# Kernel tuning notes

Measured on AMD Instinct MI355X. Metric: run time of the kernel, lower is better.

Reference implementation:

```python
import jax, jax.numpy as jnp
import numpy as np

TEMP = 0.5  # matches temperature init kwarg
EPS = 1e-12  # F.normalize eps


def _l2norm(x):
    # F.normalize(x, dim=1): x / max(||x||, eps)
    n = jnp.linalg.norm(x, axis=1, keepdims=True)
    return x / jnp.maximum(n, EPS)


def setup_inputs() -> dict:
    key = jax.random.key(0)
    k1, k2 = jax.random.split(key)
    B, D = 4096, 256
    return {
        "x_i": jax.random.normal(k1, (B, D), dtype=jnp.float32),
        "x_j": jax.random.normal(k2, (B, D), dtype=jnp.float32),
    }


def reference(x_i, x_j):
    B = x_i.shape[0]
    z = jnp.concatenate([_l2norm(x_i), _l2norm(x_j)], axis=0)  # [2B, D]
    # cosine similarity of normalized rows == matmul (avoids NxNxD broadcast)
    sim = (z @ z.T) / TEMP  # [2B, 2B]
    idx = jnp.arange(B)
    # diagonals at offsets +B and -B = positive pairs
    pos = jnp.concatenate([sim[idx, idx + B], sim[idx + B, idx]])  # [2B]
    exp_sim = jnp.exp(sim)
    # neg = all off-diagonal entries per row (neg_mask = ~eye(2B))
    exp_neg = exp_sim.sum(axis=1) - jnp.exp(jnp.diagonal(sim))  # [2B]
    exp_pos = jnp.exp(pos)
    loss = -jnp.log(exp_pos / (exp_pos + exp_neg))
    return loss.mean()
```

## Files before the change

### kernel.cpp

```cpp
#include <hip/hip_runtime.h>
#include <hip/hip_bf16.h>

typedef __attribute__((ext_vector_type(8))) short bf16x8;
typedef __attribute__((ext_vector_type(4))) float f32x4;
typedef __attribute__((ext_vector_type(4))) unsigned short ushort4v;

constexpr int BB = 4096;
constexpr int D  = 256;
constexpr int R2 = 8192;
constexpr int NSPLIT = 16;
constexpr int CT = 64;
constexpr int NT = (R2 / NSPLIT) / CT;
constexpr float SQRT2 = 1.41421356237309515f;
constexpr float E2 = 7.38905609893065f;

__device__ __forceinline__ unsigned short f2bf(float f) {
    __hip_bfloat16 h = __float2bfloat16(f);
    return *reinterpret_cast<unsigned short*>(&h);
}

__device__ __forceinline__ void async16(const unsigned short* g, unsigned short* l) {
    __builtin_amdgcn_global_load_lds(
        (const __attribute__((address_space(1))) void*)g,
        (__attribute__((address_space(3))) void*)l,
        16, 0, 0);
}

__global__ __launch_bounds__(256) void norm_kernel(const float* __restrict__ xi,
                                                   const float* __restrict__ xj,
                                                   unsigned short* __restrict__ z,
                                                   float* __restrict__ pos) {
    const int wid = threadIdx.x >> 6, lane = threadIdx.x & 63;
    const int k = blockIdx.x * 4 + wid;
    const float4* a4 = reinterpret_cast<const float4*>(xi + (size_t)k * D);
    const float4* b4 = reinterpret_cast<const float4*>(xj + (size_t)k * D);
    float4 a = a4[lane], b = b4[lane];
    float ssi = a.x*a.x + a.y*a.y + a.z*a.z + a.w*a.w;
    float ssj = b.x*b.x + b.y*b.y + b.z*b.z + b.w*b.w;
    float dot = a.x*b.x + a.y*b.y + a.z*b.z + a.w*b.w;
#pragma unroll
    for (int off = 32; off; off >>= 1) {
        ssi += __shfl_xor(ssi, off);
        ssj += __shfl_xor(ssj, off);
        dot += __shfl_xor(dot, off);
    }
    const float inv_i = 1.0f / fmaxf(sqrtf(ssi), 1e-12f);
    const float inv_j = 1.0f / fmaxf(sqrtf(ssj), 1e-12f);
    const float si = inv_i * SQRT2, sj = inv_j * SQRT2;
    ushort4v zi = { f2bf(a.x*si), f2bf(a.y*si), f2bf(a.z*si), f2bf(a.w*si) };
    ushort4v zj = { f2bf(b.x*sj), f2bf(b.y*sj), f2bf(b.z*sj), f2bf(b.w*sj) };
    *reinterpret_cast<ushort4v*>(z + (size_t)k * D + lane*4)        = zi;
    *reinterpret_cast<ushort4v*>(z + (size_t)(k+BB) * D + lane*4)   = zj;
    if (lane == 0) pos[k] = dot * inv_i * inv_j * 2.0f;
}

__global__ __launch_bounds__(256, 2) void sim_kernel(const unsigned short* __restrict__ z,
                                                     float* __restrict__ partial) {
    __shared__ unsigned short tb[2][CT * D];
    const int tid = threadIdx.x;
    const int wid = tid >> 6, lane = tid & 63;
    const int lrow = lane & 15, quad = lane >> 4;
    const int r0 = blockIdx.x * 256 + wid * 64;
    const int cbase = blockIdx.y * (R2 / NSPLIT);

    const int half = lane >> 5;
    const int srcchunk = (lane & 31) ^ (half << 2);
    const unsigned short* gstage = z + (size_t)(cbase + wid*16 + half) * D + srcchunk * 8;
    unsigned short* dst0 = &tb[0][wid * 4096];
    unsigned short* dst1 = &tb[1][wid * 4096];

#pragma unroll
    for (int i = 0; i < 8; ++i) async16(gstage + i*512, dst0 + i*512);

    bf16x8 afrag[4][8];
#pragma unroll
    for (int m = 0; m < 4; ++m)
#pragma unroll
        for (int kk = 0; kk < 8; ++kk)
            afrag[m][kk] = *reinterpret_cast<const bf16x8*>(
                z + (size_t)(r0 + m*16 + lrow) * D + kk*32 + quad*8);

    float racc[4][4];
#pragma unroll
    for (int m = 0; m < 4; ++m)
#pragma unroll
        for (int j = 0; j < 4; ++j) racc[m][j] = 0.f;

    const int r1 = lrow & 1;
    const int lb2 = (((lrow >> 1) * 512) + r1 * 256 + quad * 8) ^ (r1 * 32);

    __syncthreads();

    for (int ct = 0; ct < NT; ++ct) {
        const unsigned short* tbb = (ct & 1) ? &tb[1][0] : &tb[0][0];
        if (ct + 1 < NT) {
            const unsigned short* gs = gstage + (size_t)(ct + 1) * (CT * D);
            unsigned short* dn = (ct & 1) ? dst0 : dst1;
#pragma unroll
            for (int i = 0; i < 8; ++i) async16(gs + i*512, dn + i*512);
        }
#pragma unroll
        for (int n = 0; n < 4; ++n) {
            bf16x8 bfrag[8];
#pragma unroll
            for (int kk = 0; kk < 8; ++kk)
                bfrag[kk] = *reinterpret_cast<const bf16x8*>(&tbb[n*4096 + (lb2 ^ (kk*32))]);
#pragma unroll
            for (int m = 0; m < 4; ++m) {
                f32x4 c = {0.f, 0.f, 0.f, 0.f};
#pragma unroll
                for (int kk = 0; kk < 8; ++kk)
                    c = __builtin_amdgcn_mfma_f32_16x16x32_bf16(afrag[m][kk], bfrag[kk], c, 0, 0, 0);
#pragma unroll
                for (int j = 0; j < 4; ++j)
                    racc[m][j] += __expf(c[j]);
            }
        }
        __syncthreads();
    }

#pragma unroll
    for (int m = 0; m < 4; ++m)
#pragma unroll
        for (int j = 0; j < 4; ++j) {
            float v = racc[m][j];
            v += __shfl_xor(v, 1);
            v += __shfl_xor(v, 2);
            v += __shfl_xor(v, 4);
            v += __shfl_xor(v, 8);
            if (lrow == 0)
                partial[(size_t)blockIdx.y * R2 + r0 + m*16 + quad*4 + j] = v;
        }
}

__global__ __launch_bounds__(1024) void finalize_kernel(const float* __restrict__ partial,
                                                        const float* __restrict__ pos,
                                                        float* __restrict__ out) {
    __shared__ float wsum[16];
    const int tid = threadIdx.x;
    float lsum = 0.f;
    for (int r = tid; r < R2; r += 1024) {
        float S = 0.f;
#pragma unroll
        for (int s = 0; s < NSPLIT; ++s) S += partial[(size_t)s * R2 + r];
        const float p = pos[r & (BB - 1)];
        lsum += __logf(__expf(p) + S - E2) - p;
    }
#pragma unroll
    for (int off = 32; off; off >>= 1) lsum += __shfl_xor(lsum, off);
    if ((tid & 63) == 0) wsum[tid >> 6] = lsum;
    __syncthreads();
    if (tid == 0) {
        float t = 0.f;
#pragma unroll
        for (int i = 0; i < 16; ++i) t += wsum[i];
        out[0] = t / (float)R2;
    }
}

extern "C" void kernel_launch(void* const* d_in, const int* in_sizes, int n_in,
                              void* d_out, int out_size, void* d_ws, size_t ws_size,
                              hipStream_t stream) {
    (void)in_sizes; (void)n_in; (void)out_size; (void)ws_size;
    const float* xi = (const float*)d_in[0];
    const float* xj = (const float*)d_in[1];
    float* out = (float*)d_out;

    unsigned short* z = (unsigned short*)d_ws;
    float* partial = (float*)((char*)d_ws + (size_t)R2 * D * 2);
    float* pos     = (float*)((char*)d_ws + (size_t)R2 * D * 2 + NSPLIT*R2*4);

    norm_kernel<<<BB / 4, 256, 0, stream>>>(xi, xj, z, pos);
    sim_kernel<<<dim3(R2 / 256, NSPLIT), 256, 0, stream>>>(z, partial);
    finalize_kernel<<<1, 1024, 0, stream>>>(partial, pos, out);
}
```

Before: 102.1 us.

## Switch similarity GEMM to FP8 scaled MFMA and parallelize final reduction

Normalized embeddings are now stored as FP8 (e4m3) instead of bf16, and the similarity tile uses the 16x16x128 scaled f8f6f4 MFMA, which halves the bytes staged through LDS and cuts the MFMA count per tile. The column split grows from 16 to 32 to give more blocks. The single-block finalize becomes a multi-block reduction that accumulates into the output with atomicAdd, and the norm kernel zeroes the output first. FP8 quantization lowers the precision of the similarity logits, which are then exponentiated, so accuracy could drift. The atomic float sum also makes the result order-dependent.

```diff
diff --git a/kernel.cpp b/kernel.cpp
--- a/kernel.cpp
+++ b/kernel.cpp
@@ -1,25 +1,20 @@
 #include <hip/hip_runtime.h>
 #include <hip/hip_bf16.h>
 
-typedef __attribute__((ext_vector_type(8))) short bf16x8;
+typedef __attribute__((ext_vector_type(8))) int   i32x8;
+typedef __attribute__((ext_vector_type(4))) int   i32x4;
 typedef __attribute__((ext_vector_type(4))) float f32x4;
-typedef __attribute__((ext_vector_type(4))) unsigned short ushort4v;
 
 constexpr int BB = 4096;
 constexpr int D  = 256;
 constexpr int R2 = 8192;
-constexpr int NSPLIT = 16;
+constexpr int NSPLIT = 32;
 constexpr int CT = 64;
 constexpr int NT = (R2 / NSPLIT) / CT;
 constexpr float SQRT2 = 1.41421356237309515f;
 constexpr float E2 = 7.38905609893065f;
 
-__device__ __forceinline__ unsigned short f2bf(float f) {
-    __hip_bfloat16 h = __float2bfloat16(f);
-    return *reinterpret_cast<unsigned short*>(&h);
-}
-
-__device__ __forceinline__ void async16(const unsigned short* g, unsigned short* l) {
+__device__ __forceinline__ void async16(const unsigned char* g, unsigned char* l) {
     __builtin_amdgcn_global_load_lds(
         (const __attribute__((address_space(1))) void*)g,
         (__attribute__((address_space(3))) void*)l,
@@ -28,10 +23,12 @@
 
 __global__ __launch_bounds__(256) void norm_kernel(const float* __restrict__ xi,
                                                    const float* __restrict__ xj,
-                                                   unsigned short* __restrict__ z,
-                                                   float* __restrict__ pos) {
+                                                   int* __restrict__ z8,
+                                                   float* __restrict__ pos,
+                                                   float* __restrict__ out) {
     const int wid = threadIdx.x >> 6, lane = threadIdx.x & 63;
     const int k = blockIdx.x * 4 + wid;
+    if (blockIdx.x == 0 && threadIdx.x == 0) out[0] = 0.f;
     const float4* a4 = reinterpret_cast<const float4*>(xi + (size_t)k * D);
     const float4* b4 = reinterpret_cast<const float4*>(xj + (size_t)k * D);
     float4 a = a4[lane], b = b4[lane];
@@ -47,38 +44,38 @@
     const float inv_i = 1.0f / fmaxf(sqrtf(ssi), 1e-12f);
     const float inv_j = 1.0f / fmaxf(sqrtf(ssj), 1e-12f);
     const float si = inv_i * SQRT2, sj = inv_j * SQRT2;
-    ushort4v zi = { f2bf(a.x*si), f2bf(a.y*si), f2bf(a.z*si), f2bf(a.w*si) };
-    ushort4v zj = { f2bf(b.x*sj), f2bf(b.y*sj), f2bf(b.z*sj), f2bf(b.w*sj) };
-    *reinterpret_cast<ushort4v*>(z + (size_t)k * D + lane*4)        = zi;
-    *reinterpret_cast<ushort4v*>(z + (size_t)(k+BB) * D + lane*4)   = zj;
+    int pi = __builtin_amdgcn_cvt_pk_fp8_f32(a.x*si, a.y*si, 0, false);
+    pi     = __builtin_amdgcn_cvt_pk_fp8_f32(a.z*si, a.w*si, pi, true);
+    int pj = __builtin_amdgcn_cvt_pk_fp8_f32(b.x*sj, b.y*sj, 0, false);
+    pj     = __builtin_amdgcn_cvt_pk_fp8_f32(b.z*sj, b.w*sj, pj, true);
+    z8[(size_t)k * 64 + lane]        = pi;
+    z8[(size_t)(k + BB) * 64 + lane] = pj;
     if (lane == 0) pos[k] = dot * inv_i * inv_j * 2.0f;
 }
 
-__global__ __launch_bounds__(256, 2) void sim_kernel(const unsigned short* __restrict__ z,
+__global__ __launch_bounds__(256, 2) void sim_kernel(const unsigned char* __restrict__ z8,
                                                      float* __restrict__ partial) {
-    __shared__ unsigned short tb[2][CT * D];
+    __shared__ unsigned char tb[2][CT * D];
     const int tid = threadIdx.x;
     const int wid = tid >> 6, lane = tid & 63;
     const int lrow = lane & 15, quad = lane >> 4;
     const int r0 = blockIdx.x * 256 + wid * 64;
     const int cbase = blockIdx.y * (R2 / NSPLIT);
 
-    const int half = lane >> 5;
-    const int srcchunk = (lane & 31) ^ (half << 2);
-    const unsigned short* gstage = z + (size_t)(cbase + wid*16 + half) * D + srcchunk * 8;
-    unsigned short* dst0 = &tb[0][wid * 4096];
-    unsigned short* dst1 = &tb[1][wid * 4096];
+    const int srow = tid >> 4;
+    const unsigned char* gstage = z8 + (size_t)(cbase + srow) * D + ((tid & 15) ^ srow) * 16;
 
 #pragma unroll
-    for (int i = 0; i < 8; ++i) async16(gstage + i*512, dst0 + i*512);
+    for (int i = 0; i < 4; ++i)
+        async16(gstage + i * 16 * D, &tb[0][i * 4096 + wid * 1024]);
 
-    bf16x8 afrag[4][8];
+    i32x8 afrag[4][2];
 #pragma unroll
     for (int m = 0; m < 4; ++m)
 #pragma unroll
-        for (int kk = 0; kk < 8; ++kk)
-            afrag[m][kk] = *reinterpret_cast<const bf16x8*>(
-                z + (size_t)(r0 + m*16 + lrow) * D + kk*32 + quad*8);
+        for (int ks = 0; ks < 2; ++ks)
+            afrag[m][ks] = *reinterpret_cast<const i32x8*>(
+                z8 + (size_t)(r0 + m*16 + lrow) * D + ks*128 + quad*32);
 
     float racc[4][4];
 #pragma unroll
@@ -86,31 +83,38 @@
 #pragma unroll
         for (int j = 0; j < 4; ++j) racc[m][j] = 0.f;
 
-    const int r1 = lrow & 1;
-    const int lb2 = (((lrow >> 1) * 512) + r1 * 256 + quad * 8) ^ (r1 * 32);
-
     __syncthreads();
 
     for (int ct = 0; ct < NT; ++ct) {
-        const unsigned short* tbb = (ct & 1) ? &tb[1][0] : &tb[0][0];
+        const unsigned char* tbb = tb[ct & 1];
         if (ct + 1 < NT) {
-            const unsigned short* gs = gstage + (size_t)(ct + 1) * (CT * D);
-            unsigned short* dn = (ct & 1) ? dst0 : dst1;
+            const unsigned char* gs = gstage + (size_t)(ct + 1) * (CT * D);
+            unsigned char* dn = tb[(ct + 1) & 1];
 #pragma unroll
-            for (int i = 0; i < 8; ++i) async16(gs + i*512, dn + i*512);
+            for (int i = 0; i < 4; ++i)
+                async16(gs + i * 16 * D, dn + i * 4096 + wid * 1024);
         }
 #pragma unroll
         for (int n = 0; n < 4; ++n) {
-            bf16x8 bfrag[8];
+            const int rb = (n*16 + lrow) * D;
+            i32x8 bfrag[2];
 #pragma unroll
-            for (int kk = 0; kk < 8; ++kk)
-                bfrag[kk] = *reinterpret_cast<const bf16x8*>(&tbb[n*4096 + (lb2 ^ (kk*32))]);
+            for (int ks = 0; ks < 2; ++ks) {
+                const int pe = (ks*8 + quad*2) ^ lrow;
+                i32x4 lo = *reinterpret_cast<const i32x4*>(&tbb[rb + pe * 16]);
+                i32x4 hi = *reinterpret_cast<const i32x4*>(&tbb[rb + (pe ^ 1) * 16]);
+                bfrag[ks][0] = lo[0]; bfrag[ks][1] = lo[1];
+                bfrag[ks][2] = lo[2]; bfrag[ks][3] = lo[3];
+                bfrag[ks][4] = hi[0]; bfrag[ks][5] = hi[1];
+                bfrag[ks][6] = hi[2]; bfrag[ks][7] = hi[3];
+            }
 #pragma unroll
             for (int m = 0; m < 4; ++m) {
                 f32x4 c = {0.f, 0.f, 0.f, 0.f};
-#pragma unroll
-                for (int kk = 0; kk < 8; ++kk)
-                    c = __builtin_amdgcn_mfma_f32_16x16x32_bf16(afrag[m][kk], bfrag[kk], c, 0, 0, 0);
+                c = __builtin_amdgcn_mfma_scale_f32_16x16x128_f8f6f4(
+                        afrag[m][0], bfrag[0], c, 0, 0, 0, 127, 0, 127);
+                c = __builtin_amdgcn_mfma_scale_f32_16x16x128_f8f6f4(
+                        afrag[m][1], bfrag[1], c, 0, 0, 0, 127, 0, 127);
 #pragma unroll
                 for (int j = 0; j < 4; ++j)
                     racc[m][j] += __expf(c[j]);
@@ -133,28 +137,24 @@
         }
 }
 
-__global__ __launch_bounds__(1024) void finalize_kernel(const float* __restrict__ partial,
-                                                        const float* __restrict__ pos,
-                                                        float* __restrict__ out) {
-    __shared__ float wsum[16];
+__global__ __launch_bounds__(256) void reduce_kernel(const float* __restrict__ partial,
+                                                     const float* __restrict__ pos,
+                                                     float* __restrict__ out) {
+    __shared__ float wsum[4];
     const int tid = threadIdx.x;
-    float lsum = 0.f;
-    for (int r = tid; r < R2; r += 1024) {
-        float S = 0.f;
+    const int r = blockIdx.x * 256 + tid;
+    float S = 0.f;
 #pragma unroll
-        for (int s = 0; s < NSPLIT; ++s) S += partial[(size_t)s * R2 + r];
-        const float p = pos[r & (BB - 1)];
-        lsum += __logf(__expf(p) + S - E2) - p;
-    }
+    for (int s = 0; s < NSPLIT; ++s) S += partial[(size_t)s * R2 + r];
+    const float p = pos[r & (BB - 1)];
+    float lsum = __logf(__expf(p) + S - E2) - p;
 #pragma unroll
     for (int off = 32; off; off >>= 1) lsum += __shfl_xor(lsum, off);
     if ((tid & 63) == 0) wsum[tid >> 6] = lsum;
     __syncthreads();
     if (tid == 0) {
-        float t = 0.f;
-#pragma unroll
-        for (int i = 0; i < 16; ++i) t += wsum[i];
-        out[0] = t / (float)R2;
+        float t = wsum[0] + wsum[1] + wsum[2] + wsum[3];
+        atomicAdd(out, t * (1.0f / (float)R2));
     }
 }
 
@@ -166,11 +166,11 @@
     const float* xj = (const float*)d_in[1];
     float* out = (float*)d_out;
 
-    unsigned short* z = (unsigned short*)d_ws;
-    float* partial = (float*)((char*)d_ws + (size_t)R2 * D * 2);
-    float* pos     = (float*)((char*)d_ws + (size_t)R2 * D * 2 + NSPLIT*R2*4);
+    unsigned char* z8 = (unsigned char*)d_ws;
+    float* partial = (float*)((char*)d_ws + (size_t)R2 * D);
+    float* pos     = (float*)((char*)d_ws + (size_t)R2 * D + (size_t)NSPLIT*R2*4);
 
-    norm_kernel<<<BB / 4, 256, 0, stream>>>(xi, xj, z, pos);
-    sim_kernel<<<dim3(R2 / 256, NSPLIT), 256, 0, stream>>>(z, partial);
-    finalize_kernel<<<1, 1024, 0, stream>>>(partial, pos, out);
+    norm_kernel<<<BB / 4, 256, 0, stream>>>(xi, xj, (int*)z8, pos, out);
+    sim_kernel<<<dim3(R2 / 256, NSPLIT), 256, 0, stream>>>(z8, partial);
+    reduce_kernel<<<NSPLIT, 256, 0, stream>>>(partial, pos, out);
 }
```

Result: slower. 180.5 us (+76.9%).
